# Kernel optimization log

Measured on AMD Instinct MI355X. Metric: run time of the kernel, lower is better.

The kernel has to match this reference:

```python
import jax, jax.numpy as jnp
import numpy as np
from jax import lax

N, K, T_OBS, PRED = 64, 48, 30, 15
EMB, NODE, EDGE, ATT, CNN = 64, 128, 256, 64, 512


def setup_inputs():
    key = jax.random.key(0)
    ks = jax.random.split(key, 18)
    rn = lambda k, s, sc=1.0: jax.random.normal(k, s, jnp.float32) * sc
    return {
        "img_embedding": rn(ks[0], (N, CNN)),
        "target_obs_pos_abs": rn(ks[1], (N, T_OBS, 2)),
        "target_obs_pos_rel": rn(ks[2], (N, T_OBS, 2)),
        "target_obs_pos_step": rn(ks[3], (N, T_OBS, 2), 0.1),
        "nearby_obs_pos_abs": rn(ks[4], (N, K, T_OBS, 2)),
        "nearby_obs_pos_rel": rn(ks[5], (N, K, T_OBS, 2)),
        "nearby_obs_pos_step": rn(ks[6], (N, K, T_OBS, 2), 0.1),
        "target_obs_hist_size": jax.random.randint(ks[7], (N, 1), 0, T_OBS),
        "nearby_obs_hist_sizes": jax.random.randint(ks[8], (N, K, 1), 0, T_OBS),
        "W_disp": rn(ks[9], (EMB, 2), 0.1), "b_disp": jnp.zeros((EMB,), jnp.float32),
        "Wih_t": rn(ks[10], (4 * NODE, EMB), 0.05), "Whh_t": rn(ks[11], (4 * NODE, NODE), 0.05),
        "bih_t": jnp.zeros((4 * NODE,), jnp.float32), "bhh_t": jnp.zeros((4 * NODE,), jnp.float32),
        "Wih_n": rn(ks[12], (4 * EDGE, EMB), 0.05), "Whh_n": rn(ks[13], (4 * EDGE, EDGE), 0.05),
        "bih_n": jnp.zeros((4 * EDGE,), jnp.float32), "bhh_n": jnp.zeros((4 * EDGE,), jnp.float32),
        "W_att_t": rn(ks[14], (ATT, 2), 0.1), "b_att_t": jnp.zeros((ATT,), jnp.float32),
        "W_att_n": rn(ks[15], (ATT, 2), 0.1), "b_att_n": jnp.zeros((ATT,), jnp.float32),
        "W_pred": rn(ks[16], (2, NODE + CNN + EDGE), 0.02), "b_pred": jnp.zeros((2,), jnp.float32),
    }


def _lstm_cell(x, h, c, Wih, Whh, bih, bhh):
    # PyTorch LSTM gate order: i, f, g, o
    g = x @ Wih.T + h @ Whh.T + bih + bhh
    i, f, gg, o = jnp.split(g, 4, axis=-1)
    c2 = jax.nn.sigmoid(f) * c + jax.nn.sigmoid(i) * jnp.tanh(gg)
    return jax.nn.sigmoid(o) * jnp.tanh(c2), c2


def _forward(img_embedding, target_obs_pos_abs, target_obs_pos_rel, target_obs_pos_step,
             nearby_obs_pos_abs, nearby_obs_pos_rel, nearby_obs_pos_step,
             W_disp, b_disp, Wih_t, Whh_t, bih_t, bhh_t, Wih_n, Whh_n, bih_n, bhh_n,
             W_att_t, b_att_t, W_att_n, b_att_n, W_pred, b_pred,
             target_obs_hist_size, nearby_obs_hist_sizes):
    t_hist = target_obs_hist_size[:, 0]          # [N]
    n_hist = nearby_obs_hist_sizes[:, :, 0]      # [N, K]
    M = N * K

    def step(carry, t):
        tht, tct, nht, nct, Ht, cabs, crel, cstep, nabs, nstep = carry
        is_obs = t < T_OBS
        tc = jnp.minimum(t, T_OBS - 1)
        # prediction branch (only takes effect when t >= T_OBS)
        pred_out = jnp.concatenate([tht, img_embedding, Ht], 1) @ W_pred.T + b_pred  # [N,2]
        cabs = jnp.where(is_obs, target_obs_pos_abs[:, tc], cabs + pred_out)
        crel = jnp.where(is_obs, target_obs_pos_rel[:, tc], crel + pred_out)
        cstep = jnp.where(is_obs, target_obs_pos_step[:, tc], pred_out)
        nabs = jnp.where(is_obs, nearby_obs_pos_abs[:, :, tc], nabs)
        nstep = jnp.where(is_obs, nearby_obs_pos_step[:, :, tc], nstep)
        tmask = jnp.where(is_obs, t_hist > T_OBS - t, True)   # [N] bool
        nmask = jnp.where(is_obs, n_hist > T_OBS - t, True)   # [N,K] bool
        gate_t = jnp.sum(tmask) > 0  # emulates 'continue' when no target observed
        # target LSTM step, masked scatter-back
        th2, tc2 = _lstm_cell(cstep @ W_disp.T + b_disp, tht, tct, Wih_t, Whh_t, bih_t, bhh_t)
        u = (tmask & gate_t)[:, None]
        tht = jnp.where(u, th2, tht)
        tct = jnp.where(u, tc2, tct)
        # nearby LSTM step, masked scatter-back
        currN = jnp.sum(nmask)
        gate_n = gate_t & (currN > 0)
        nh2, nc2 = _lstm_cell(nstep.reshape(M, 2) @ W_disp.T + b_disp, nht, nct, Wih_n, Whh_n, bih_n, bhh_n)
        un = (nmask.reshape(M) & gate_n)[:, None]
        nht = jnp.where(un, nh2, nht)
        nct = jnp.where(un, nc2, nct)
        # social attention over padded nearby dim
        an = (nabs - cabs[:, None, :]) @ W_att_n.T + b_att_n   # [N,K,ATT]
        at = crel @ W_att_t.T + b_att_t                        # [N,ATT]
        mf = nmask.astype(jnp.float32)
        sc = jnp.einsum('nka,na->nk', an, at) * currN.astype(jnp.float32) / jnp.sqrt(jnp.float32(ATT))
        sc = sc * mf
        num = jnp.exp(sc - jnp.max(sc, 1, keepdims=True)) * mf
        w = num / (jnp.sum(num, 1, keepdims=True) + 1e-6)
        Ht = jnp.where(gate_n, jnp.einsum('nke,nk->ne', nht.reshape(N, K, EDGE), w), Ht)
        return (tht, tct, nht, nct, Ht, cabs, crel, cstep, nabs, nstep), crel

    z = lambda s: jnp.zeros(s, jnp.float32)
    init = (z((N, NODE)), z((N, NODE)), z((M, EDGE)), z((M, EDGE)), z((N, EDGE)),
            z((N, 2)), z((N, 2)), z((N, 2)), z((N, K, 2)), z((N, K, 2)))
    _, rels = lax.scan(step, init, jnp.arange(1, T_OBS + PRED))
    # last PRED emitted crel values are pred_traj[:, 0:PRED]
    return jnp.transpose(rels[-PRED:], (1, 0, 2))


def reference(img_embedding, target_obs_pos_abs, target_obs_pos_rel, target_obs_pos_step,
              nearby_obs_pos_abs, nearby_obs_pos_rel, nearby_obs_pos_step,
              target_obs_hist_size, nearby_obs_hist_sizes,
              W_disp, b_disp, Wih_t, Whh_t, bih_t, bhh_t, Wih_n, Whh_n, bih_n, bhh_n,
              W_att_t, b_att_t, W_att_n, b_att_n, W_pred, b_pred):
    return _forward(img_embedding, target_obs_pos_abs, target_obs_pos_rel, target_obs_pos_step,
                    nearby_obs_pos_abs, nearby_obs_pos_rel, nearby_obs_pos_step,
                    W_disp, b_disp, Wih_t, Whh_t, bih_t, bhh_t, Wih_n, Whh_n, bih_n, bhh_n,
                    W_att_t, b_att_t, W_att_n, b_att_n, W_pred, b_pred,
                    target_obs_hist_size, nearby_obs_hist_sizes)
```

## Files before the change

### kernel.cpp

```cpp
#include <hip/hip_runtime.h>
#include <math.h>

#define NT 64
#define KN 48
#define TOBS 30
#define NPRED 15
#define EMB 64
#define NODE 128
#define EDGE 256
#define ATTD 64
#define CNN 512
#define GNN 1024
#define GTT 512
#define KKA 320
#define TMAX 44

typedef _Float16 f16;
typedef f16 f16x8 __attribute__((ext_vector_type(8)));
typedef f16 f16x2 __attribute__((ext_vector_type(2)));
typedef float f32x4 __attribute__((ext_vector_type(4)));

__device__ __forceinline__ float rcp_f(float x) { return __builtin_amdgcn_rcpf(x); }
__device__ __forceinline__ float sigm(float x) { return rcp_f(1.f + __expf(-x)); }
__device__ __forceinline__ float tanh_f(float x) {
  float xx = fminf(fmaxf(x, -20.f), 20.f);
  float e = __expf(-2.f * xx);
  return (1.f - e) * rcp_f(1.f + e);
}
__device__ __forceinline__ unsigned ldcoh(const unsigned* p) {
  return __hip_atomic_load(p, __ATOMIC_RELAXED, __HIP_MEMORY_SCOPE_AGENT);
}
__device__ __forceinline__ float ldcohf(const float* p) {
  unsigned u = __hip_atomic_load((const unsigned*)p, __ATOMIC_RELAXED, __HIP_MEMORY_SCOPE_AGENT);
  return __builtin_bit_cast(float, u);
}
__device__ __forceinline__ void stcoh(unsigned* p, unsigned v) {
  __hip_atomic_store(p, v, __ATOMIC_RELAXED, __HIP_MEMORY_SCOPE_AGENT);
}
__device__ __forceinline__ void stcohf(float* p, float v) {
  __hip_atomic_store((unsigned*)p, __builtin_bit_cast(unsigned, v),
                     __ATOMIC_RELAXED, __HIP_MEMORY_SCOPE_AGENT);
}

__global__ __launch_bounds__(512) void prep_kernel(
    const float* __restrict__ Wih_n, const float* __restrict__ Whh_n,
    const float* __restrict__ bih_n, const float* __restrict__ bhh_n,
    const float* __restrict__ Wih_t, const float* __restrict__ Whh_t,
    const float* __restrict__ bih_t, const float* __restrict__ bhh_t,
    const int* __restrict__ t_hist, const int* __restrict__ n_hist,
    f16* __restrict__ Wn, f16* __restrict__ Wt,
    float* __restrict__ bias_n, float* __restrict__ bias_t,
    int* __restrict__ gt_arr, int* __restrict__ gn_arr, float* __restrict__ cn_arr,
    int* __restrict__ last29p, unsigned* __restrict__ flags)
{
  const int gid = blockIdx.x * 512 + threadIdx.x;
  const int nthr = gridDim.x * 512;
  __shared__ int sgn[TMAX + 1];

  if (gid < 2 * NT) flags[gid] = 0u;

  for (int idx = gid; idx < GNN * KKA; idx += nthr) {
    const int j    = idx & 7;
    const int lane = (idx >> 3) & 63;
    const int g    = (idx >> 9) & 3;
    const int r    = idx >> 11;
    const int kk   = r % 10;
    const int s    = r / 10;
    const int w    = s & 7;
    const int h    = s >> 3;
    const int col = g * 256 + h * 128 + w * 16 + (lane & 15);
    const int k   = kk * 32 + (lane >> 4) * 8 + j;
    const float v = (k < EMB) ? Wih_n[col * EMB + k] : Whh_n[col * EDGE + (k - EMB)];
    Wn[idx] = (f16)v;
  }
  for (int idx = gid; idx < GTT * 192; idx += nthr) {
    const int j = idx & 7;
    const int col = (idx >> 3) & 511;
    const int c8 = idx >> 12;
    const int k = c8 * 8 + j;
    const float v = (k < EMB) ? Wih_t[col * EMB + k] : Whh_t[col * NODE + (k - EMB)];
    Wt[idx] = (f16)v;
  }
  for (int idx = gid; idx < GNN; idx += nthr) bias_n[idx] = bih_n[idx] + bhh_n[idx];
  for (int idx = gid; idx < GTT; idx += nthr) bias_t[idx] = bih_t[idx] + bhh_t[idx];

  if (blockIdx.x == 0 && threadIdx.x < 352) {
    const int t = (threadIdx.x >> 3) + 1;
    const int part = threadIdx.x & 7;
    int any_t = 0, cnt = 0;
    if (t < TOBS) {
      const int thr = TOBS - t;
      for (int nn = part; nn < NT; nn += 8) any_t |= (t_hist[nn] > thr) ? 1 : 0;
      for (int m = part; m < NT * KN; m += 8) cnt += (n_hist[m] > thr) ? 1 : 0;
    } else { any_t = (part == 0); cnt = (part == 0) ? NT * KN : 0; }
    #pragma unroll
    for (int off = 1; off < 8; off <<= 1) {
      any_t |= __shfl_xor(any_t, off);
      cnt   += __shfl_xor(cnt, off);
    }
    if (part == 0) {
      const int gn = (any_t && cnt > 0) ? 1 : 0;
      gt_arr[t] = any_t;
      gn_arr[t] = gn;
      cn_arr[t] = (float)cnt;
      sgn[t] = gn;
    }
  }
  __syncthreads();
  if (blockIdx.x == 0 && threadIdx.x == 0) {
    int l = 30;
    for (int t = 29; t >= 1; --t) if (sgn[t]) { l = t; break; }
    last29p[0] = l;
  }
}

__global__ __launch_bounds__(512, 2) void model_kernel(
    const float* __restrict__ img, const float* __restrict__ tabs,
    const float* __restrict__ trel, const float* __restrict__ tstep,
    const float* __restrict__ nabs_g, const float* __restrict__ nstep_g,
    const int* __restrict__ thist_g, const int* __restrict__ nhist_g,
    const float* __restrict__ W_disp, const float* __restrict__ b_disp,
    const float* __restrict__ W_att_t, const float* __restrict__ b_att_t,
    const float* __restrict__ W_att_n, const float* __restrict__ b_att_n,
    const float* __restrict__ W_pred, const float* __restrict__ b_pred,
    const f16* __restrict__ Wn, const f16* __restrict__ Wt,
    const float* __restrict__ bias_n, const float* __restrict__ bias_t,
    const int* __restrict__ gt_arr, const int* __restrict__ gn_arr,
    const float* __restrict__ cn_arr, const int* __restrict__ last29p,
    unsigned* __restrict__ flags, unsigned* __restrict__ Hglob,
    float* __restrict__ Tglob,
    float* __restrict__ out)
{
  __shared__ f16 s_wlds[3 * 16384];
  __shared__ f16 Ax[KN][72];
  __shared__ f16 Ah[KN][264];
  __shared__ float s_tht[NODE];
  __shared__ float s_tct[64];
  __shared__ f16  s_th16[NODE];
  __shared__ float s_Ht[EDGE];
  __shared__ f16  s_x16[EMB];
  __shared__ float s_g[256];
  __shared__ float s_bt[256];
  __shared__ float s_at[ATTD];
  __shared__ float s_sc[KN], s_w[KN];
  __shared__ float s_scal[8];
  __shared__ float s_pimg[2];
  __shared__ int   s_nh[KN];
  __shared__ float s_wp[2][384];
  __shared__ float s_wan0[ATTD], s_wan1[ATTD], s_ban[ATTD];
  __shared__ float s_wat0[ATTD], s_wat1[ATTD], s_bat[ATTD];
  __shared__ float s_wd0[EMB], s_wd1[EMB], s_bd[EMB];

  const int tid  = threadIdx.x;
  const int n    = blockIdx.x & 63;
  const int hb   = blockIdx.x >> 6;
  const int w    = tid >> 6;
  const int lane = tid & 63;
  const int cl   = lane & 15;
  const int kq   = lane >> 4;
  const int koff = kq * 8;

  for (int i = tid; i < KN * 264; i += 512) ((f16*)Ah)[i] = (f16)0.f;
  for (int i = tid; i < NODE; i += 512) { s_tht[i] = 0.f; s_th16[i] = (f16)0.f; }
  if (tid < 64) s_tct[tid] = 0.f;
  for (int i = tid; i < EDGE; i += 512) s_Ht[i] = 0.f;
  if (tid < 256) {
    const int g = tid >> 6, dl = tid & 63;
    s_bt[tid] = bias_t[g * 128 + hb * 64 + dl];
  }
  for (int i = tid; i < 768; i += 512) {
    const int ww = i / 384, j = i - ww * 384;
    s_wp[ww][j] = (j < 128) ? W_pred[ww * 896 + j] : W_pred[ww * 896 + 640 + (j - 128)];
  }
  if (tid < KN) s_nh[tid] = nhist_g[n * KN + tid];
  if (tid < 8) s_scal[tid] = 0.f;
  if (tid >= 64 && tid < 128) {
    const int a = tid - 64;
    s_wan0[a] = W_att_n[a * 2]; s_wan1[a] = W_att_n[a * 2 + 1]; s_ban[a] = b_att_n[a];
  }
  if (tid >= 128 && tid < 192) {
    const int a = tid - 128;
    s_wat0[a] = W_att_t[a * 2]; s_wat1[a] = W_att_t[a * 2 + 1]; s_bat[a] = b_att_t[a];
  }
  if (tid >= 192 && tid < 256) {
    const int e = tid - 192;
    s_wd0[e] = W_disp[e * 2]; s_wd1[e] = W_disp[e * 2 + 1]; s_bd[e] = b_disp[e];
  }
  const int thist = thist_g[n];
  const int last29 = last29p[0];

  for (int i = tid; i < 3 * 8 * 256; i += 512) {
    const int c  = i & 255;
    const int wv = (i >> 8) & 7;
    const int kk = i >> 11;
    const size_t gbase = ((size_t)((hb * 8 + wv) * 10 + kk)) * 2048;
    *(f16x8*)(s_wlds + (size_t)(kk * 8 + wv) * 2048 + c * 8) =
        *(const f16x8*)(Wn + gbase + c * 8);
  }

  if (w < 2) {
    float s = 0.f;
    for (int j = lane; j < CNN; j += 64) s += img[n * CNN + j] * W_pred[w * 896 + 128 + j];
    for (int off = 32; off; off >>= 1) s += __shfl_down(s, off);
    if (lane == 0) s_pimg[w] = s + b_pred[w];
  }

  float creg[3][4];
  #pragma unroll
  for (int b = 0; b < 3; ++b)
    #pragma unroll
    for (int c = 0; c < 4; ++c) creg[b][c] = 0.f;

  float bias_q[4];
  #pragma unroll
  for (int g = 0; g < 4; ++g) bias_q[g] = bias_n[g * 256 + hb * 128 + w * 16 + cl];

  const f16* gW = Wn + ((size_t)(hb * 8 + w) * 10) * 2048 + (size_t)lane * 8;
  const f16* lW = s_wlds + (size_t)w * 2048 + (size_t)lane * 8;
  const int e_g = hb * 128 + w * 16 + cl;
  unsigned* myflag = flags + n * 2 + hb;
  unsigned* otflag = flags + n * 2 + (1 - hb);
  int bn = 0;

  __syncthreads();

  {
    for (int i = tid; i < KN * EMB; i += 512) {
      const int k = i >> 6, e = i & 63;
      const float s0 = nstep_g[((n * KN + k) * TOBS + 1) * 2 + 0];
      const float s1 = nstep_g[((n * KN + k) * TOBS + 1) * 2 + 1];
      Ax[k][e] = (f16)(s0 * s_wd0[e] + s1 * s_wd1[e] + s_bd[e]);
    }
    if (tid < 2) {
      s_scal[tid]     = tabs[(n * TOBS + 1) * 2 + tid];
      s_scal[2 + tid] = trel[(n * TOBS + 1) * 2 + tid];
      s_scal[4 + tid] = tstep[(n * TOBS + 1) * 2 + tid];
    }
    if (tid >= 448) {
      const int e = tid - 448;
      const float a0 = tstep[(n * TOBS + 1) * 2 + 0], a1 = tstep[(n * TOBS + 1) * 2 + 1];
      s_x16[e] = (f16)(a0 * s_wd0[e] + a1 * s_wd1[e] + s_bd[e]);
    }
    if (tid >= 384 && tid < 448) {
      const int a = tid - 384;
      const float r0 = trel[(n * TOBS + 1) * 2 + 0], r1 = trel[(n * TOBS + 1) * 2 + 1];
      s_at[a] = r0 * s_wat0[a] + r1 * s_wat1[a] + s_bat[a];
    }
  }
  __syncthreads();

  for (int t = 1; t <= TMAX; ++t) {
    const bool is_obs = (t < TOBS);
    const int tc = is_obs ? t : (TOBS - 1);
    const int gate_t = gt_arr[t];
    const int gate_n = gn_arr[t];
    const float currN = cn_arr[t];
    const bool tmask = is_obs ? (thist > (TOBS - t)) : true;
    const bool do_t = gate_t && tmask;
    const bool need_x = (gate_n || do_t);
    const bool do_att = gate_n && (t >= last29);
    const int par = bn & 1;

    if (!is_obs) {
      if (w < 2) {
        float s = 0.f;
        for (int j = lane; j < NODE; j += 64) s += s_tht[j] * s_wp[w][j];
        for (int j = lane; j < EDGE; j += 64) s += s_Ht[j] * s_wp[w][128 + j];
        for (int off = 32; off; off >>= 1) s += __shfl_down(s, off);
        if (lane == 0) {
          const float p = s + s_pimg[w];
          const float cabs = s_scal[w] + p;
          const float crel = s_scal[2 + w] + p;
          s_scal[w] = cabs; s_scal[2 + w] = crel; s_scal[4 + w] = p;
          if (hb == 0) out[(n * NPRED + (t - TOBS)) * 2 + w] = crel;
        }
      }
      __syncthreads();
      if (tid >= 448) {
        const int e = tid - 448;
        s_x16[e] = (f16)(s_scal[4] * s_wd0[e] + s_scal[5] * s_wd1[e] + s_bd[e]);
      }
      if (tid >= 384 && tid < 448) {
        const int a = tid - 384;
        s_at[a] = s_scal[2] * s_wat0[a] + s_scal[3] * s_wat1[a] + s_bat[a];
      }
      __syncthreads();
    }

    f16 hreg[3][4];
    if (gate_n) {
      f32x4 acc[3][4];
      #pragma unroll
      for (int rt = 0; rt < 3; ++rt)
        #pragma unroll
        for (int g = 0; g < 4; ++g) acc[rt][g] = (f32x4){0.f, 0.f, 0.f, 0.f};

      #pragma unroll
      for (int kk = 0; kk < 10; ++kk) {
        f16x8 bf[4];
        if (kk < 3) {
          #pragma unroll
          for (int g = 0; g < 4; ++g)
            bf[g] = *(const f16x8*)(lW + kk * 16384 + g * 512);
        } else {
          #pragma unroll
          for (int g = 0; g < 4; ++g)
            bf[g] = *(const f16x8*)(gW + kk * 2048 + g * 512);
        }
        f16x8 af[3];
        #pragma unroll
        for (int rt = 0; rt < 3; ++rt) {
          const int row = rt * 16 + cl;
          const f16* ap = (kk < 2) ? &Ax[row][kk * 32 + koff]
                                   : &Ah[row][(kk - 2) * 32 + koff];
          af[rt] = *(const f16x8*)ap;
        }
        #pragma unroll
        for (int g = 0; g < 4; ++g)
          #pragma unroll
          for (int rt = 0; rt < 3; ++rt)
            acc[rt][g] = __builtin_amdgcn_mfma_f32_16x16x32_f16(af[rt], bf[g], acc[rt][g], 0, 0, 0);
      }

      unsigned* Hg = Hglob + (size_t)(par * NT + n) * (KN * 128);
      #pragma unroll
      for (int rt = 0; rt < 3; ++rt) {
        #pragma unroll
        for (int jj = 0; jj < 4; ++jj) {
          const int row = rt * 16 + kq * 4 + jj;
          const bool nm = is_obs ? (s_nh[row] > (TOBS - t)) : true;
          f16 hv;
          if (nm) {
            const float iv = acc[rt][0][jj] + bias_q[0];
            const float fv = acc[rt][1][jj] + bias_q[1];
            const float gv = acc[rt][2][jj] + bias_q[2];
            const float ov = acc[rt][3][jj] + bias_q[3];
            const float c2 = sigm(fv) * creg[rt][jj] + sigm(iv) * tanh_f(gv);
            creg[rt][jj] = c2;
            hv = (f16)(sigm(ov) * tanh_f(c2));
          } else {
            hv = Ah[row][e_g];
          }
          hreg[rt][jj] = hv;
          const unsigned lo = (unsigned)__builtin_bit_cast(unsigned short, hv);
          const unsigned hi = (unsigned)__shfl_down((int)lo, 1);
          if (!(cl & 1))
            stcoh(Hg + row * 128 + (e_g >> 1), lo | (hi << 16));
        }
      }
    }

    if (do_t && tid < 256) {
      const int g = tid >> 6, dl = tid & 63;
      const int col = g * 128 + hb * 64 + dl;
      float gg = s_bt[tid];
      const f16x2* xt2 = (const f16x2*)s_x16;
      const f16x2* th2 = (const f16x2*)s_th16;
      const f16x8* wp = (const f16x8*)(Wt + col * 8);
      #pragma unroll
      for (int c8 = 0; c8 < 8; ++c8) {
        const f16x8 wv = wp[c8 * 512];
        #pragma unroll
        for (int j2 = 0; j2 < 4; ++j2) {
          f16x2 wpair = {wv[2 * j2], wv[2 * j2 + 1]};
          gg = __builtin_amdgcn_fdot2(wpair, xt2[c8 * 4 + j2], gg, false);
        }
      }
      #pragma unroll
      for (int c8 = 8; c8 < 24; ++c8) {
        const f16x8 wv = wp[c8 * 512];
        #pragma unroll
        for (int j2 = 0; j2 < 4; ++j2) {
          f16x2 wpair = {wv[2 * j2], wv[2 * j2 + 1]};
          gg = __builtin_amdgcn_fdot2(wpair, th2[(c8 - 8) * 4 + j2], gg, false);
        }
      }
      s_g[tid] = gg;
    }
    if (do_att && tid >= 256 && tid < 256 + KN) {
      const int k = tid - 256;
      const float a0 = nabs_g[((n * KN + k) * TOBS + tc) * 2 + 0] - s_scal[0];
      const float a1 = nabs_g[((n * KN + k) * TOBS + tc) * 2 + 1] - s_scal[1];
      const bool nm = is_obs ? (s_nh[k] > (TOBS - t)) : true;
      float sc = 0.f;
      for (int a = 0; a < ATTD; ++a)
        sc += (a0 * s_wan0[a] + a1 * s_wan1[a] + s_ban[a]) * s_at[a];
      sc *= currN * 0.125f;
      s_sc[k] = nm ? sc : 0.f;
      s_w[k]  = nm ? 1.f : 0.f;
    }
    __syncthreads();

    if (do_t && tid < 64) {
      const int d = hb * 64 + tid;
      const float iv = s_g[tid], fv = s_g[64 + tid];
      const float gv = s_g[128 + tid], ov = s_g[192 + tid];
      const float c2 = sigm(fv) * s_tct[tid] + sigm(iv) * tanh_f(gv);
      s_tct[tid] = c2;
      const float nh = sigm(ov) * tanh_f(c2);
      s_tht[d] = nh;
      s_th16[d] = (f16)nh;
      stcohf(Tglob + ((size_t)(par * NT + n) * 2 + hb) * 64 + tid, nh);
    }
    if (do_att && w == 4) {
      const bool act = lane < KN;
      const float sc = act ? s_sc[lane] : -1.0e30f;
      const float mf = act ? s_w[lane] : 0.f;
      float mx = sc;
      #pragma unroll
      for (int off = 32; off; off >>= 1) mx = fmaxf(mx, __shfl_xor(mx, off));
      float num = __expf(sc - mx) * mf;
      float sum = num;
      #pragma unroll
      for (int off = 32; off; off >>= 1) sum += __shfl_xor(sum, off);
      if (act) s_w[lane] = num * rcp_f(sum + 1e-6f);
    }
    __syncthreads();

    if (need_x && tid == 0) {
      stcoh(myflag, (unsigned)(bn + 1));
    }

    {
      const int tn = t + 1;
      if (tn <= TOBS) {
        const int tcn = (tn < TOBS) ? tn : (TOBS - 1);
        for (int i = tid; i < KN * EMB; i += 512) {
          const int k = i >> 6, e = i & 63;
          const float s0 = nstep_g[((n * KN + k) * TOBS + tcn) * 2 + 0];
          const float s1 = nstep_g[((n * KN + k) * TOBS + tcn) * 2 + 1];
          Ax[k][e] = (f16)(s0 * s_wd0[e] + s1 * s_wd1[e] + s_bd[e]);
        }
      }
      if (tn < TOBS) {
        if (tid < 2) {
          s_scal[tid]     = tabs[(n * TOBS + tn) * 2 + tid];
          s_scal[2 + tid] = trel[(n * TOBS + tn) * 2 + tid];
          s_scal[4 + tid] = tstep[(n * TOBS + tn) * 2 + tid];
        }
        if (tid >= 448) {
          const int e = tid - 448;
          const float a0 = tstep[(n * TOBS + tn) * 2 + 0], a1 = tstep[(n * TOBS + tn) * 2 + 1];
          s_x16[e] = (f16)(a0 * s_wd0[e] + a1 * s_wd1[e] + s_bd[e]);
        }
        if (tid >= 384 && tid < 448) {
          const int a = tid - 384;
          const float r0 = trel[(n * TOBS + tn) * 2 + 0], r1 = trel[(n * TOBS + tn) * 2 + 1];
          s_at[a] = r0 * s_wat0[a] + r1 * s_wat1[a] + s_bat[a];
        }
      }
    }

    if (need_x && tid == 0) {
      const unsigned step = (unsigned)(bn + 1);
      while (ldcoh(otflag) < step)
        __builtin_amdgcn_s_sleep(2);
    }
    __syncthreads();

    if (gate_n) {
      const unsigned* Hg = Hglob + (size_t)(par * NT + n) * (KN * 128);
      const int ob = (1 - hb) * 64;
      for (int i = tid; i < KN * 64; i += 512) {
        const int row = i >> 6, c = i & 63;
        const unsigned v = ldcoh(Hg + row * 128 + ob + c);
        *(unsigned*)&Ah[row][(ob + c) * 2] = v;
      }
      #pragma unroll
      for (int rt = 0; rt < 3; ++rt)
        #pragma unroll
        for (int jj = 0; jj < 4; ++jj)
          Ah[rt * 16 + kq * 4 + jj][e_g] = hreg[rt][jj];
    }
    if (do_t && tid >= 448) {
      const int dl = tid - 448;
      const int d = (1 - hb) * 64 + dl;
      const float nh = ldcohf(Tglob + ((size_t)(par * NT + n) * 2 + (1 - hb)) * 64 + dl);
      s_tht[d] = nh;
      s_th16[d] = (f16)nh;
    }
    __syncthreads();

    if (do_att && tid < EDGE) {
      float h = 0.f;
      for (int k = 0; k < KN; ++k) h += (float)Ah[k][tid] * s_w[k];
      s_Ht[tid] = h;
    }
    if (need_x) bn++;
    if (t >= 29) __syncthreads();
  }
}

extern "C" void kernel_launch(void* const* d_in, const int* in_sizes, int n_in,
                              void* d_out, int out_size, void* d_ws, size_t ws_size,
                              hipStream_t stream) {
  const float* img    = (const float*)d_in[0];
  const float* tabs   = (const float*)d_in[1];
  const float* trel   = (const float*)d_in[2];
  const float* tstep  = (const float*)d_in[3];
  const float* nabs   = (const float*)d_in[4];
  const float* nstep  = (const float*)d_in[6];
  const int*   thist  = (const int*)d_in[7];
  const int*   nhist  = (const int*)d_in[8];
  const float* W_disp = (const float*)d_in[9];
  const float* b_disp = (const float*)d_in[10];
  const float* Wih_t  = (const float*)d_in[11];
  const float* Whh_t  = (const float*)d_in[12];
  const float* bih_t  = (const float*)d_in[13];
  const float* bhh_t  = (const float*)d_in[14];
  const float* Wih_n  = (const float*)d_in[15];
  const float* Whh_n  = (const float*)d_in[16];
  const float* bih_n  = (const float*)d_in[17];
  const float* bhh_n  = (const float*)d_in[18];
  const float* W_att_t = (const float*)d_in[19];
  const float* b_att_t = (const float*)d_in[20];
  const float* W_att_n = (const float*)d_in[21];
  const float* b_att_n = (const float*)d_in[22];
  const float* W_pred  = (const float*)d_in[23];
  const float* b_pred  = (const float*)d_in[24];

  char* ws = (char*)d_ws;
  f16*      Wn      = (f16*)(ws);
  f16*      Wt      = (f16*)(ws + 655360);
  float*    bias_n  = (float*)(ws + 851968);
  float*    bias_t  = (float*)(ws + 856064);
  int*      gt_arr  = (int*)(ws + 858112);
  int*      gn_arr  = (int*)(ws + 858304);
  float*    cn_arr  = (float*)(ws + 858496);
  int*      last29p = (int*)(ws + 859648);
  unsigned* flags   = (unsigned*)(ws + 860160);
  unsigned* Hglob   = (unsigned*)(ws + 1048576);
  float*    Tglob   = (float*)(ws + 4194304);

  prep_kernel<<<64, 512, 0, stream>>>(Wih_n, Whh_n, bih_n, bhh_n, Wih_t, Whh_t,
                                      bih_t, bhh_t, thist, nhist, Wn, Wt,
                                      bias_n, bias_t, gt_arr, gn_arr, cn_arr,
                                      last29p, flags);
  model_kernel<<<2 * NT, 512, 0, stream>>>(img, tabs, trel, tstep, nabs, nstep,
                                           thist, nhist, W_disp, b_disp,
                                           W_att_t, b_att_t, W_att_n, b_att_n,
                                           W_pred, b_pred,
                                           Wn, Wt, bias_n, bias_t,
                                           gt_arr, gn_arr, cn_arr, last29p,
                                           flags, Hglob, Tglob,
                                           (float*)d_out);
}
```

Before: 716.9 us.

## Overlap cross-block hidden-state exchange with MFMA and compute target LSTM redundantly

Each of the two blocks that share an agent now computes the full 128-wide target LSTM itself instead of splitting it and exchanging halves through global memory. The edge LSTM no longer waits for the partner block at the end of every step. It orders the K-loop so the block's own half of the hidden state is consumed first, waits on the partner's flag only before the remote half, and reads that half straight from global memory via coherent 64-bit loads. The full Ah copy is assembled only when attention needs it. The aim is to take a barrier and a spin-wait off the per-step critical path, at the cost of redundant target-LSTM work, uncached global operand loads inside the MFMA loop, and a larger Hglob zero-fill in the prep kernel.

```diff
diff --git a/kernel.cpp b/kernel.cpp
--- a/kernel.cpp
+++ b/kernel.cpp
@@ -30,16 +30,11 @@
 __device__ __forceinline__ unsigned ldcoh(const unsigned* p) {
   return __hip_atomic_load(p, __ATOMIC_RELAXED, __HIP_MEMORY_SCOPE_AGENT);
 }
-__device__ __forceinline__ float ldcohf(const float* p) {
-  unsigned u = __hip_atomic_load((const unsigned*)p, __ATOMIC_RELAXED, __HIP_MEMORY_SCOPE_AGENT);
-  return __builtin_bit_cast(float, u);
+__device__ __forceinline__ unsigned long long ldcoh64(const unsigned long long* p) {
+  return __hip_atomic_load(p, __ATOMIC_RELAXED, __HIP_MEMORY_SCOPE_AGENT);
 }
 __device__ __forceinline__ void stcoh(unsigned* p, unsigned v) {
   __hip_atomic_store(p, v, __ATOMIC_RELAXED, __HIP_MEMORY_SCOPE_AGENT);
-}
-__device__ __forceinline__ void stcohf(float* p, float v) {
-  __hip_atomic_store((unsigned*)p, __builtin_bit_cast(unsigned, v),
-                     __ATOMIC_RELAXED, __HIP_MEMORY_SCOPE_AGENT);
 }
 
 __global__ __launch_bounds__(512) void prep_kernel(
@@ -51,13 +46,15 @@
     f16* __restrict__ Wn, f16* __restrict__ Wt,
     float* __restrict__ bias_n, float* __restrict__ bias_t,
     int* __restrict__ gt_arr, int* __restrict__ gn_arr, float* __restrict__ cn_arr,
-    int* __restrict__ last29p, unsigned* __restrict__ flags)
+    int* __restrict__ last29p, unsigned* __restrict__ flags,
+    unsigned* __restrict__ Hglob)
 {
   const int gid = blockIdx.x * 512 + threadIdx.x;
   const int nthr = gridDim.x * 512;
   __shared__ int sgn[TMAX + 1];
 
   if (gid < 2 * NT) flags[gid] = 0u;
+  for (int idx = gid; idx < 2 * NT * KN * 128; idx += nthr) Hglob[idx] = 0u;
 
   for (int idx = gid; idx < GNN * KKA; idx += nthr) {
     const int j    = idx & 7;
@@ -128,19 +125,18 @@
     const int* __restrict__ gt_arr, const int* __restrict__ gn_arr,
     const float* __restrict__ cn_arr, const int* __restrict__ last29p,
     unsigned* __restrict__ flags, unsigned* __restrict__ Hglob,
-    float* __restrict__ Tglob,
     float* __restrict__ out)
 {
   __shared__ f16 s_wlds[3 * 16384];
   __shared__ f16 Ax[KN][72];
   __shared__ f16 Ah[KN][264];
   __shared__ float s_tht[NODE];
-  __shared__ float s_tct[64];
+  __shared__ float s_tct[NODE];
   __shared__ f16  s_th16[NODE];
   __shared__ float s_Ht[EDGE];
   __shared__ f16  s_x16[EMB];
-  __shared__ float s_g[256];
-  __shared__ float s_bt[256];
+  __shared__ float s_g[GTT];
+  __shared__ float s_bt[GTT];
   __shared__ float s_at[ATTD];
   __shared__ float s_sc[KN], s_w[KN];
   __shared__ float s_scal[8];
@@ -161,13 +157,11 @@
   const int koff = kq * 8;
 
   for (int i = tid; i < KN * 264; i += 512) ((f16*)Ah)[i] = (f16)0.f;
-  for (int i = tid; i < NODE; i += 512) { s_tht[i] = 0.f; s_th16[i] = (f16)0.f; }
-  if (tid < 64) s_tct[tid] = 0.f;
+  for (int i = tid; i < NODE; i += 512) {
+    s_tht[i] = 0.f; s_tct[i] = 0.f; s_th16[i] = (f16)0.f;
+  }
   for (int i = tid; i < EDGE; i += 512) s_Ht[i] = 0.f;
-  if (tid < 256) {
-    const int g = tid >> 6, dl = tid & 63;
-    s_bt[tid] = bias_t[g * 128 + hb * 64 + dl];
-  }
+  for (int i = tid; i < GTT; i += 512) s_bt[i] = bias_t[i];
   for (int i = tid; i < 768; i += 512) {
     const int ww = i / 384, j = i - ww * 384;
     s_wp[ww][j] = (j < 128) ? W_pred[ww * 896 + j] : W_pred[ww * 896 + 640 + (j - 128)];
@@ -192,9 +186,10 @@
   for (int i = tid; i < 3 * 8 * 256; i += 512) {
     const int c  = i & 255;
     const int wv = (i >> 8) & 7;
-    const int kk = i >> 11;
-    const size_t gbase = ((size_t)((hb * 8 + wv) * 10 + kk)) * 2048;
-    *(f16x8*)(s_wlds + (size_t)(kk * 8 + wv) * 2048 + c * 8) =
+    const int u  = i >> 11;
+    const int kkg = (u < 2) ? u : (2 + hb * 4);
+    const size_t gbase = ((size_t)((hb * 8 + wv) * 10 + kkg)) * 2048;
+    *(f16x8*)(s_wlds + (size_t)(u * 8 + wv) * 2048 + c * 8) =
         *(const f16x8*)(Wn + gbase + c * 8);
   }
 
@@ -220,7 +215,7 @@
   const int e_g = hb * 128 + w * 16 + cl;
   unsigned* myflag = flags + n * 2 + hb;
   unsigned* otflag = flags + n * 2 + (1 - hb);
-  int bn = 0;
+  int hn = 0;
 
   __syncthreads();
 
@@ -257,9 +252,8 @@
     const float currN = cn_arr[t];
     const bool tmask = is_obs ? (thist > (TOBS - t)) : true;
     const bool do_t = gate_t && tmask;
-    const bool need_x = (gate_n || do_t);
     const bool do_att = gate_n && (t >= last29);
-    const int par = bn & 1;
+    const bool ah_full = (t > last29);
 
     if (!is_obs) {
       if (w < 2) {
@@ -289,6 +283,9 @@
 
     f16 hreg[3][4];
     if (gate_n) {
+      const int prv = (hn - 1) & 1;
+      const int par = hn & 1;
+      const unsigned* HgR = Hglob + (size_t)(prv * NT + n) * (KN * 128);
       f32x4 acc[3][4];
       #pragma unroll
       for (int rt = 0; rt < 3; ++rt)
@@ -296,24 +293,39 @@
         for (int g = 0; g < 4; ++g) acc[rt][g] = (f32x4){0.f, 0.f, 0.f, 0.f};
 
       #pragma unroll
-      for (int kk = 0; kk < 10; ++kk) {
+      for (int u = 0; u < 10; ++u) {
+        const int kkg = (u < 2) ? u
+                      : (u < 6) ? (2 + hb * 4 + (u - 2))
+                                : (2 + (1 - hb) * 4 + (u - 6));
         f16x8 bf[4];
-        if (kk < 3) {
+        if (u < 3) {
           #pragma unroll
           for (int g = 0; g < 4; ++g)
-            bf[g] = *(const f16x8*)(lW + kk * 16384 + g * 512);
+            bf[g] = *(const f16x8*)(lW + u * 16384 + g * 512);
         } else {
           #pragma unroll
           for (int g = 0; g < 4; ++g)
-            bf[g] = *(const f16x8*)(gW + kk * 2048 + g * 512);
+            bf[g] = *(const f16x8*)(gW + kkg * 2048 + g * 512);
+        }
+        if (u == 6 && !ah_full) {
+          while (ldcoh(otflag) < (unsigned)hn) __builtin_amdgcn_s_sleep(1);
         }
         f16x8 af[3];
         #pragma unroll
         for (int rt = 0; rt < 3; ++rt) {
           const int row = rt * 16 + cl;
-          const f16* ap = (kk < 2) ? &Ax[row][kk * 32 + koff]
-                                   : &Ah[row][(kk - 2) * 32 + koff];
-          af[rt] = *(const f16x8*)ap;
+          if (u < 2) {
+            af[rt] = *(const f16x8*)&Ax[row][u * 32 + koff];
+          } else if (u < 6 || ah_full) {
+            af[rt] = *(const f16x8*)&Ah[row][(kkg - 2) * 32 + koff];
+          } else {
+            const unsigned long long* pq = (const unsigned long long*)
+                ((const char*)HgR + (size_t)row * 512 + ((kkg - 2) * 32 + koff) * 2);
+            union { unsigned long long q[2]; f16x8 v; } uu;
+            uu.q[0] = ldcoh64(pq);
+            uu.q[1] = ldcoh64(pq + 1);
+            af[rt] = uu.v;
+          }
         }
         #pragma unroll
         for (int g = 0; g < 4; ++g)
@@ -322,7 +334,7 @@
             acc[rt][g] = __builtin_amdgcn_mfma_f32_16x16x32_f16(af[rt], bf[g], acc[rt][g], 0, 0, 0);
       }
 
-      unsigned* Hg = Hglob + (size_t)(par * NT + n) * (KN * 128);
+      unsigned* HgW = Hglob + (size_t)(par * NT + n) * (KN * 128);
       #pragma unroll
       for (int rt = 0; rt < 3; ++rt) {
         #pragma unroll
@@ -345,18 +357,16 @@
           const unsigned lo = (unsigned)__builtin_bit_cast(unsigned short, hv);
           const unsigned hi = (unsigned)__shfl_down((int)lo, 1);
           if (!(cl & 1))
-            stcoh(Hg + row * 128 + (e_g >> 1), lo | (hi << 16));
-        }
-      }
-    }
-
-    if (do_t && tid < 256) {
-      const int g = tid >> 6, dl = tid & 63;
-      const int col = g * 128 + hb * 64 + dl;
+            stcoh(HgW + row * 128 + (e_g >> 1), lo | (hi << 16));
+        }
+      }
+    }
+
+    if (do_t) {
       float gg = s_bt[tid];
       const f16x2* xt2 = (const f16x2*)s_x16;
       const f16x2* th2 = (const f16x2*)s_th16;
-      const f16x8* wp = (const f16x8*)(Wt + col * 8);
+      const f16x8* wp = (const f16x8*)(Wt + tid * 8);
       #pragma unroll
       for (int c8 = 0; c8 < 8; ++c8) {
         const f16x8 wv = wp[c8 * 512];
@@ -389,18 +399,23 @@
       s_sc[k] = nm ? sc : 0.f;
       s_w[k]  = nm ? 1.f : 0.f;
     }
-    __syncthreads();
-
-    if (do_t && tid < 64) {
-      const int d = hb * 64 + tid;
-      const float iv = s_g[tid], fv = s_g[64 + tid];
-      const float gv = s_g[128 + tid], ov = s_g[192 + tid];
+    if (gate_n || do_t) __syncthreads();
+
+    if (gate_n) {
+      #pragma unroll
+      for (int rt = 0; rt < 3; ++rt)
+        #pragma unroll
+        for (int jj = 0; jj < 4; ++jj)
+          Ah[rt * 16 + kq * 4 + jj][e_g] = hreg[rt][jj];
+    }
+    if (do_t && tid < NODE) {
+      const float iv = s_g[tid], fv = s_g[NODE + tid];
+      const float gv = s_g[2 * NODE + tid], ov = s_g[3 * NODE + tid];
       const float c2 = sigm(fv) * s_tct[tid] + sigm(iv) * tanh_f(gv);
       s_tct[tid] = c2;
       const float nh = sigm(ov) * tanh_f(c2);
-      s_tht[d] = nh;
-      s_th16[d] = (f16)nh;
-      stcohf(Tglob + ((size_t)(par * NT + n) * 2 + hb) * 64 + tid, nh);
+      s_tht[tid] = nh;
+      s_th16[tid] = (f16)nh;
     }
     if (do_att && w == 4) {
       const bool act = lane < KN;
@@ -415,18 +430,17 @@
       for (int off = 32; off; off >>= 1) sum += __shfl_xor(sum, off);
       if (act) s_w[lane] = num * rcp_f(sum + 1e-6f);
     }
-    __syncthreads();
-
-    if (need_x && tid == 0) {
-      stcoh(myflag, (unsigned)(bn + 1));
-    }
+    if (gate_n || do_t) __syncthreads();
+
+    if (gate_n && t < TMAX && tid == 0)
+      stcoh(myflag, (unsigned)(hn + 1));
 
     {
       const int tn = t + 1;
       if (tn <= TOBS) {
-        const int tcn = (tn < TOBS) ? tn : (TOBS - 1);
         for (int i = tid; i < KN * EMB; i += 512) {
           const int k = i >> 6, e = i & 63;
+          const int tcn = (tn < TOBS) ? tn : (TOBS - 1);
           const float s0 = nstep_g[((n * KN + k) * TOBS + tcn) * 2 + 0];
           const float s1 = nstep_g[((n * KN + k) * TOBS + tcn) * 2 + 1];
           Ax[k][e] = (f16)(s0 * s_wd0[e] + s1 * s_wd1[e] + s_bd[e]);
@@ -451,43 +465,24 @@
       }
     }
 
-    if (need_x && tid == 0) {
-      const unsigned step = (unsigned)(bn + 1);
-      while (ldcoh(otflag) < step)
-        __builtin_amdgcn_s_sleep(2);
-    }
-    __syncthreads();
-
-    if (gate_n) {
-      const unsigned* Hg = Hglob + (size_t)(par * NT + n) * (KN * 128);
+    if (do_att && t < TMAX) {
+      while (ldcoh(otflag) < (unsigned)(hn + 1)) __builtin_amdgcn_s_sleep(1);
+      const unsigned* HgP = Hglob + (size_t)((hn & 1) * NT + n) * (KN * 128);
       const int ob = (1 - hb) * 64;
       for (int i = tid; i < KN * 64; i += 512) {
         const int row = i >> 6, c = i & 63;
-        const unsigned v = ldcoh(Hg + row * 128 + ob + c);
+        const unsigned v = ldcoh(HgP + row * 128 + ob + c);
         *(unsigned*)&Ah[row][(ob + c) * 2] = v;
       }
-      #pragma unroll
-      for (int rt = 0; rt < 3; ++rt)
-        #pragma unroll
-        for (int jj = 0; jj < 4; ++jj)
-          Ah[rt * 16 + kq * 4 + jj][e_g] = hreg[rt][jj];
-    }
-    if (do_t && tid >= 448) {
-      const int dl = tid - 448;
-      const int d = (1 - hb) * 64 + dl;
-      const float nh = ldcohf(Tglob + ((size_t)(par * NT + n) * 2 + (1 - hb)) * 64 + dl);
-      s_tht[d] = nh;
-      s_th16[d] = (f16)nh;
-    }
+      __syncthreads();
+      if (tid < EDGE) {
+        float h = 0.f;
+        for (int k = 0; k < KN; ++k) h += (float)Ah[k][tid] * s_w[k];
+        s_Ht[tid] = h;
+      }
+    }
+    if (gate_n) hn++;
     __syncthreads();
-
-    if (do_att && tid < EDGE) {
-      float h = 0.f;
-      for (int k = 0; k < KN; ++k) h += (float)Ah[k][tid] * s_w[k];
-      s_Ht[tid] = h;
-    }
-    if (need_x) bn++;
-    if (t >= 29) __syncthreads();
   }
 }
 
@@ -530,18 +525,17 @@
   int*      last29p = (int*)(ws + 859648);
   unsigned* flags   = (unsigned*)(ws + 860160);
   unsigned* Hglob   = (unsigned*)(ws + 1048576);
-  float*    Tglob   = (float*)(ws + 4194304);
 
   prep_kernel<<<64, 512, 0, stream>>>(Wih_n, Whh_n, bih_n, bhh_n, Wih_t, Whh_t,
                                       bih_t, bhh_t, thist, nhist, Wn, Wt,
                                       bias_n, bias_t, gt_arr, gn_arr, cn_arr,
-                                      last29p, flags);
+                                      last29p, flags, Hglob);
   model_kernel<<<2 * NT, 512, 0, stream>>>(img, tabs, trel, tstep, nabs, nstep,
                                            thist, nhist, W_disp, b_disp,
                                            W_att_t, b_att_t, W_att_n, b_att_n,
                                            W_pred, b_pred,
                                            Wn, Wt, bias_n, bias_t,
                                            gt_arr, gn_arr, cn_arr, last29p,
-                                           flags, Hglob, Tglob,
+                                           flags, Hglob,
                                            (float*)d_out);
 }
```

After: 763.6 us. +6.5%, slower.
